# Kernel optimization log

Hardware: AMD Instinct MI355X
Metric: run time of the kernel (lower is better)

The kernel has to match this reference:

```python
import jax, jax.numpy as jnp
import numpy as np

NUM_CLASSES = 21
THRESH = 0.5
NEGPOS = 3
VAR0, VAR1 = 0.1, 0.2
FEAT = 19
N_ANCH = 9
B = 256
NUM_OBJS = 12
P = FEAT * FEAT * N_ANCH  # 3249


def make_priors():
    # 19x19 grid, 3 scales x 3 aspect ratios (1, 2, 1/2) -> 9 anchors/cell, center form
    cxy = (np.arange(FEAT, dtype=np.float32) + 0.5) / FEAT
    cx, cy = np.meshgrid(cxy, cxy, indexing='ij')  # [19,19]
    scales = np.array([0.1, 0.2, 0.35], dtype=np.float32)
    ratios = np.array([1.0, 2.0, 0.5], dtype=np.float32)
    w = (scales[:, None] * np.sqrt(ratios)[None, :]).reshape(-1)  # [9]
    h = (scales[:, None] / np.sqrt(ratios)[None, :]).reshape(-1)
    cx = np.broadcast_to(cx[:, :, None], (FEAT, FEAT, N_ANCH))
    cy = np.broadcast_to(cy[:, :, None], (FEAT, FEAT, N_ANCH))
    w = np.broadcast_to(w[None, None, :], (FEAT, FEAT, N_ANCH))
    h = np.broadcast_to(h[None, None, :], (FEAT, FEAT, N_ANCH))
    pri = np.stack([cx, cy, w, h], axis=-1).reshape(-1, 4)
    return jnp.asarray(np.clip(pri, 1e-3, 1.0))


def setup_inputs() -> dict:
    key = jax.random.key(0)
    k1, k2, k3, k4, k5 = jax.random.split(key, 5)
    loc_data = jax.random.normal(k1, (B, P, 4), dtype=jnp.float32)
    conf_data = jax.random.normal(k2, (B, P, NUM_CLASSES), dtype=jnp.float32)
    priors = make_priors()
    xy = jax.random.uniform(k3, (B, NUM_OBJS, 2), minval=0.05, maxval=0.65)
    wh = jax.random.uniform(k4, (B, NUM_OBJS, 2), minval=0.05, maxval=0.30)
    labels = jax.random.randint(k5, (B, NUM_OBJS), 0, NUM_CLASSES - 1).astype(jnp.float32)
    targets = jnp.concatenate([xy, xy + wh, labels[..., None]], axis=-1)  # [B,O,5]
    return {"loc_data": loc_data, "conf_data": conf_data, "priors": priors, "targets": targets}


def point_form(boxes):  # (cx,cy,w,h) -> (x1,y1,x2,y2)
    return jnp.concatenate([boxes[:, :2] - boxes[:, 2:] / 2,
                            boxes[:, :2] + boxes[:, 2:] / 2], axis=1)


def jaccard(a, b):  # a: [n,4], b: [m,4] point form -> [n,m]
    lt = jnp.maximum(a[:, None, :2], b[None, :, :2])
    rb = jnp.minimum(a[:, None, 2:], b[None, :, 2:])
    inter = jnp.prod(jnp.clip(rb - lt, 0.0, None), axis=-1)
    area_a = jnp.prod(a[:, 2:] - a[:, :2], axis=-1)
    area_b = jnp.prod(b[:, 2:] - b[:, :2], axis=-1)
    return inter / (area_a[:, None] + area_b[None, :] - inter)


def encode(matched, priors):  # matched point-form [P,4], priors center-form [P,4]
    g_cxcy = ((matched[:, :2] + matched[:, 2:]) / 2 - priors[:, :2]) / (VAR0 * priors[:, 2:])
    g_wh = jnp.log((matched[:, 2:] - matched[:, :2]) / priors[:, 2:]) / VAR1
    return jnp.concatenate([g_cxcy, g_wh], axis=1)


def match_one(truths, labels, priors, priors_pt):
    overlaps = jaccard(truths, priors_pt)          # [O,P]
    best_prior_idx = jnp.argmax(overlaps, axis=1)  # [O]
    best_truth_ov = jnp.max(overlaps, axis=0)      # [P]
    best_truth_idx = jnp.argmax(overlaps, axis=0)  # [P]
    best_truth_ov = best_truth_ov.at[best_prior_idx].set(2.0)
    best_truth_idx = best_truth_idx.at[best_prior_idx].set(jnp.arange(truths.shape[0]))
    matches = truths[best_truth_idx]               # [P,4]
    conf = labels[best_truth_idx] + 1
    conf = jnp.where(best_truth_ov < THRESH, 0, conf)
    return encode(matches, priors), conf


def reference(loc_data, conf_data, priors, targets):
    truths = targets[:, :, :4]
    labels = targets[:, :, 4].astype(jnp.int32)
    priors_pt = point_form(priors)
    loc_t, conf_t = jax.vmap(lambda t, l: match_one(t, l, priors, priors_pt))(truths, labels)
    loc_t = jax.lax.stop_gradient(loc_t)
    conf_t = jax.lax.stop_gradient(conf_t)

    pos = conf_t > 0                                               # [B,P]
    # smooth L1 (sum) over matched priors
    d = loc_data - loc_t
    ad = jnp.abs(d)
    sl1 = jnp.where(ad < 1.0, 0.5 * d * d, ad - 0.5)
    loss_l = jnp.sum(sl1 * pos[..., None].astype(sl1.dtype))

    # per-prior CE = logsumexp - logit[target]
    lse = jax.nn.logsumexp(conf_data, axis=-1)                     # [B,P]
    gathered = jnp.take_along_axis(conf_data, conf_t[..., None], axis=2)[..., 0]
    ce = lse - gathered                                            # [B,P]

    # hard negative mining: double argsort rank of neg losses
    loss_c_mine = jnp.where(pos, 0.0, ce)
    loss_idx = jnp.argsort(-loss_c_mine, axis=1)
    idx_rank = jnp.argsort(loss_idx, axis=1)
    num_pos = jnp.sum(pos, axis=1, keepdims=True)                  # [B,1]
    num_neg = jnp.minimum(NEGPOS * num_pos, P - 1)
    neg = idx_rank < num_neg

    sel = pos | neg
    loss_c = jnp.sum(jnp.where(sel, ce, 0.0))

    have_centerloss = jnp.max(sel.reshape(B, FEAT, FEAT, N_ANCH), axis=3).reshape(-1)
    conf_t_featuremap = jnp.max(conf_t.reshape(B, FEAT, FEAT, N_ANCH), axis=3).reshape(-1)

    N = jnp.sum(num_pos).astype(loc_data.dtype)
    return loss_l / N, loss_c / N, conf_t_featuremap, have_centerloss
```

## Files before the change

### kernel.cpp

```cpp
#include <hip/hip_runtime.h>
#include <math.h>

#pragma clang fp contract(off)

#define BB      256
#define PP      3249
#define NCLS    21
#define NOBJ    12
#define CELLS   361
#define CH      13
#define THRESH_ 0.5f

typedef float vf4 __attribute__((ext_vector_type(4), aligned(4)));
typedef float vrec __attribute__((ext_vector_type(4)));


struct Row { vf4 a, b, c, d, e; float f; };

__device__ __forceinline__ Row load_row(const float* cd) {
    const vf4* q = (const vf4*)cd;
    Row r;
    r.a = q[0]; r.b = q[1]; r.c = q[2]; r.d = q[3]; r.e = q[4];
    r.f = cd[20];
    return r;
}

__device__ __forceinline__ float lse21(const Row& r) {
    float m = r.a[0];
    m = fmaxf(m, r.a[1]); m = fmaxf(m, r.a[2]); m = fmaxf(m, r.a[3]);
    m = fmaxf(m, r.b[0]); m = fmaxf(m, r.b[1]); m = fmaxf(m, r.b[2]); m = fmaxf(m, r.b[3]);
    m = fmaxf(m, r.c[0]); m = fmaxf(m, r.c[1]); m = fmaxf(m, r.c[2]); m = fmaxf(m, r.c[3]);
    m = fmaxf(m, r.d[0]); m = fmaxf(m, r.d[1]); m = fmaxf(m, r.d[2]); m = fmaxf(m, r.d[3]);
    m = fmaxf(m, r.e[0]); m = fmaxf(m, r.e[1]); m = fmaxf(m, r.e[2]); m = fmaxf(m, r.e[3]);
    m = fmaxf(m, r.f);
    float s = 0.0f;
    s += expf(r.a[0]-m); s += expf(r.a[1]-m); s += expf(r.a[2]-m); s += expf(r.a[3]-m);
    s += expf(r.b[0]-m); s += expf(r.b[1]-m); s += expf(r.b[2]-m); s += expf(r.b[3]-m);
    s += expf(r.c[0]-m); s += expf(r.c[1]-m); s += expf(r.c[2]-m); s += expf(r.c[3]-m);
    s += expf(r.d[0]-m); s += expf(r.d[1]-m); s += expf(r.d[2]-m); s += expf(r.d[3]-m);
    s += expf(r.e[0]-m); s += expf(r.e[1]-m); s += expf(r.e[2]-m); s += expf(r.e[3]-m);
    s += expf(r.f-m);
    return logf(s) + m;
}

template <int NBITS>
__device__ __forceinline__ void agg_add(int* hist, bool active, unsigned bin, int lane) {
    unsigned long long mm = __ballot(active);
#pragma unroll
    for (int bit = 0; bit < NBITS; ++bit) {
        unsigned long long bb = __ballot(active && ((bin >> bit) & 1));
        mm &= ((bin >> bit) & 1) ? bb : ~bb;
    }
    if (active && (__ffsll(mm) - 1 == lane))
        atomicAdd(&hist[bin], (int)__popcll(mm));
}

__device__ __forceinline__ void pick_bin(const int* hist, int nbins, int kv, int lane,
                                         int* s_chosen, int* s_knext, int* s_cnt) {
    const int per = (nbins >= 64) ? (nbins >> 6) : 1;
    const int base = lane * per;
    int ls = 0;
    if (base < nbins)
        for (int k = 0; k < per; ++k) ls += hist[base + k];
    int x = ls;
#pragma unroll
    for (int off = 1; off < 64; off <<= 1) {
        int y = __shfl_down(x, off);
        if (lane + off < 64) x += y;
    }
    int cum = x - ls;
    if (base < nbins) {
        for (int k = per - 1; k >= 0; --k) {
            int h = hist[base + k];
            if (cum < kv && kv <= cum + h) { *s_chosen = base + k; *s_knext = kv - cum; *s_cnt = h; }
            cum += h;
        }
    }
}

__global__ __launch_bounds__(256, 6) void prep_kernel(
    const float* __restrict__ conf, const float* __restrict__ priors,
    const float* __restrict__ targets, vrec* __restrict__ recs,
    unsigned long long* __restrict__ pt)
{
    const int chunk = blockIdx.x, b = blockIdx.y;
    const int tid = threadIdx.x, lane = tid & 63, wid = tid >> 6;
    const int p = chunk * 256 + tid;
    const bool valid = (p < PP);

    __shared__ float s_tx1[NOBJ], s_ty1[NOBJ], s_tx2[NOBJ], s_ty2[NOBJ], s_area[NOBJ];
    __shared__ unsigned long long s_wk[NOBJ][4];

    if (tid < NOBJ) {
        const float* t = targets + ((size_t)b * NOBJ + tid) * 5;
        float x1 = t[0], y1 = t[1], x2 = t[2], y2 = t[3];
        s_tx1[tid] = x1; s_ty1[tid] = y1; s_tx2[tid] = x2; s_ty2[tid] = y2;
        s_area[tid] = (x2 - x1) * (y2 - y1);
    }
    __syncthreads();

    vf4 pr = {0.0f, 0.0f, 0.0f, 0.0f};
    if (valid) pr = *(const vf4*)(priors + 4 * p);
    float px1 = pr[0] - pr[2] / 2.0f, py1 = pr[1] - pr[3] / 2.0f;
    float px2 = pr[0] + pr[2] / 2.0f, py2 = pr[1] + pr[3] / 2.0f;
    float area_p = (px2 - px1) * (py2 - py1);

    float bov = -1.0f; int bidx = 0;
#pragma unroll
    for (int j = 0; j < NOBJ; ++j) {
        float ltx = fmaxf(s_tx1[j], px1);
        float lty = fmaxf(s_ty1[j], py1);
        float rbx = fminf(s_tx2[j], px2);
        float rby = fminf(s_ty2[j], py2);
        float iw = fmaxf(rbx - ltx, 0.0f);
        float ih = fmaxf(rby - lty, 0.0f);
        float inter = iw * ih;
        float iou = inter / ((s_area[j] + area_p) - inter);
        if (iou > bov) { bov = iou; bidx = j; }
        unsigned long long k = valid
            ? (((unsigned long long)__float_as_uint(iou) << 32) | (0xFFFFFFFFu - (unsigned)p))
            : 0ull;
#pragma unroll
        for (int off = 32; off > 0; off >>= 1) {
            unsigned long long k2 = __shfl_xor(k, off);
            if (k2 > k) k = k2;
        }
        if (lane == 0) s_wk[j][wid] = k;
    }

    if (valid) {
        Row r = load_row(conf + ((size_t)b * PP + p) * NCLS);
        float lse = lse21(r);
        vrec rec;
        rec[0] = bov; rec[1] = __int_as_float(bidx); rec[2] = lse; rec[3] = r.a[0];
        recs[(size_t)b * PP + p] = rec;
    }
    __syncthreads();
    if (tid < NOBJ) {
        unsigned long long m = s_wk[tid][0];
#pragma unroll
        for (int w2 = 1; w2 < 4; ++w2) { unsigned long long v = s_wk[tid][w2]; if (v > m) m = v; }
        pt[((size_t)b * CH + chunk) * NOBJ + tid] = m;
    }
}

__global__ __launch_bounds__(1024, 4) void select_kernel(
    const float* __restrict__ loc, const float* __restrict__ conf,
    const float* __restrict__ priors, const float* __restrict__ targets,
    const vrec* __restrict__ recs, const unsigned long long* __restrict__ pt,
    int* __restrict__ numpos, double* __restrict__ lossl,
    double* __restrict__ lossc, float* __restrict__ out)
{
    const int b = blockIdx.x, tid = threadIdx.x;
    const int lane = tid & 63, wid = tid >> 6;

    __shared__ float s_tx1[NOBJ], s_ty1[NOBJ], s_tx2[NOBJ], s_ty2[NOBJ];
    __shared__ int   s_label[NOBJ], s_bpi[NOBJ];
    __shared__ unsigned s_key[PP];
    __shared__ float s_ce[PP];
    __shared__ unsigned char s_ct[PP];
    __shared__ int s_hist[2][256];
    __shared__ int s_chosen, s_knext, s_cnt, s_nneg;
    __shared__ double s_pl[16];
    __shared__ int    s_pn[16];
    __shared__ double s_pc[16];

    const vrec* rb = recs + (size_t)b * PP;
    vrec r0 = rb[tid];
    vrec r1 = rb[tid + 1024];
    vrec r2 = rb[tid + 2048];
    const bool h3 = (tid + 3072 < PP);
    vrec r3; if (h3) r3 = rb[tid + 3072];

    if (tid < NOBJ) {
        const float* t = targets + ((size_t)b * NOBJ + tid) * 5;
        s_tx1[tid] = t[0]; s_ty1[tid] = t[1]; s_tx2[tid] = t[2]; s_ty2[tid] = t[3];
        s_label[tid] = (int)t[4];
        const unsigned long long* q = pt + (size_t)b * CH * NOBJ + tid;
        unsigned long long m = q[0];
#pragma unroll
        for (int c2 = 1; c2 < CH; ++c2) {
            unsigned long long v = q[(size_t)c2 * NOBJ];
            if (v > m) m = v;
        }
        s_bpi[tid] = (int)(0xFFFFFFFFu - (unsigned)(m & 0xFFFFFFFFull));
    }
    for (int k = tid; k < 512; k += 1024) ((int*)s_hist)[k] = 0;
    __syncthreads();

    int bpi[NOBJ];
#pragma unroll
    for (int j = 0; j < NOBJ; ++j) bpi[j] = s_bpi[j];

    int my_pos = 0;
    double my_lossl = 0.0;
    const float* confb = conf + (size_t)b * PP * NCLS;

    auto body = [&](vrec r, int p) {
        float bov = r[0]; int bidx = __float_as_int(r[1]);
        float lse = r[2]; float c0 = r[3];
        int jov = -1;
#pragma unroll
        for (int j = 0; j < NOBJ; ++j) if (bpi[j] == p) jov = j;
        int idx; float ov;
        if (jov >= 0) { idx = jov; ov = 2.0f; }
        else          { idx = bidx; ov = bov; }
        int c = (ov < THRESH_) ? 0 : (s_label[idx] + 1);
        s_ct[p] = (unsigned char)c;

        float cdc = (c == 0) ? c0 : confb[(size_t)p * NCLS + c];
        float ce  = lse - cdc;
        s_ce[p] = ce;
        float v = (c > 0) ? 0.0f : ce;
        s_key[p] = __float_as_uint(v);

        if (c > 0) {
            ++my_pos;
            vf4 prr = *(const vf4*)(priors + 4 * p);
            float m0 = s_tx1[idx], m1 = s_ty1[idx], m2 = s_tx2[idx], m3 = s_ty2[idx];
            float g0 = ((m0 + m2) / 2.0f - prr[0]) / (0.1f * prr[2]);
            float g1 = ((m1 + m3) / 2.0f - prr[1]) / (0.1f * prr[3]);
            float g2 = logf((m2 - m0) / prr[2]) / 0.2f;
            float g3 = logf((m3 - m1) / prr[3]) / 0.2f;
            const float* ld = loc + ((size_t)b * PP + p) * 4;
            float d0 = ld[0] - g0, d1 = ld[1] - g1, d2 = ld[2] - g2, d3 = ld[3] - g3;
            float a0 = fabsf(d0), a1 = fabsf(d1), a2 = fabsf(d2), a3 = fabsf(d3);
            my_lossl += (double)((a0 < 1.0f) ? 0.5f * d0 * d0 : a0 - 0.5f);
            my_lossl += (double)((a1 < 1.0f) ? 0.5f * d1 * d1 : a1 - 0.5f);
            my_lossl += (double)((a2 < 1.0f) ? 0.5f * d2 * d2 : a2 - 0.5f);
            my_lossl += (double)((a3 < 1.0f) ? 0.5f * d3 * d3 : a3 - 0.5f);
        }
    };
    body(r0, tid); body(r1, tid + 1024); body(r2, tid + 2048);
    if (h3) body(r3, tid + 3072);

#pragma unroll
    for (int off = 32; off > 0; off >>= 1) {
        my_lossl += __shfl_down(my_lossl, off);
        my_pos   += __shfl_down(my_pos, off);
    }
    if (lane == 0) { s_pl[wid] = my_lossl; s_pn[wid] = my_pos; }
    __syncthreads();
    if (tid == 0) {
        double L = 0.0; int n = 0;
#pragma unroll
        for (int w2 = 0; w2 < 16; ++w2) { L += s_pl[w2]; n += s_pn[w2]; }
        lossl[b] = L; numpos[b] = n;
        s_nneg = min(3 * n, PP - 1);
    }

    unsigned prefix = 0u, pmask = 0u;
    int ptie = 0x7FFFFFFF;
    bool done = false;
    const int shifts[4] = {24, 16, 8, 0};
#pragma unroll
    for (int r = 0; r < 4; ++r) {
        if (!done) {
            const int sh = shifts[r];
            int* hist = s_hist[r & 1];
            for (int i = tid; i < PP; i += 1024) {
                unsigned key = s_key[i];
                agg_add<8>(hist, (key & pmask) == prefix, (key >> sh) & 0xFFu, lane);
            }
            __syncthreads();
            if (tid < 64) pick_bin(hist, 256, (r == 0) ? s_nneg : s_knext, lane,
                                   &s_chosen, &s_knext, &s_cnt);
            else { for (int k = tid - 64; k < 256; k += 960) s_hist[(r + 1) & 1][k] = 0; }
            __syncthreads();
            prefix |= ((unsigned)s_chosen) << sh;
            pmask  |= 0xFFu << sh;
            if (s_cnt == 1) done = true;
        }
    }

    if (!done && s_knext < s_cnt) {
        int* hist = s_hist[0];
        for (int i = tid; i < PP; i += 1024)
            agg_add<8>(hist, s_key[i] == prefix, ((4095u - (unsigned)i) >> 4) & 0xFFu, lane);
        __syncthreads();
        if (tid < 64) pick_bin(hist, 256, s_knext, lane, &s_chosen, &s_knext, &s_cnt);
        else { for (int k = tid - 64; k < 256; k += 960) s_hist[1][k] = 0; }
        __syncthreads();
        const int binA = s_chosen;
        int* hist2 = s_hist[1];
        for (int i = tid; i < PP; i += 1024) {
            unsigned hi = 4095u - (unsigned)i;
            agg_add<4>(hist2, (s_key[i] == prefix) && (((hi >> 4) & 0xFFu) == (unsigned)binA),
                       hi & 0xFu, lane);
        }
        __syncthreads();
        if (tid < 64) pick_bin(hist2, 16, s_knext, lane, &s_chosen, &s_knext, &s_cnt);
        __syncthreads();
        ptie = 4095 - ((binA << 4) | s_chosen);
    }

    double my_c = 0.0;
    for (int cI = tid; cI < CELLS; cI += 1024) {
        int mc = 0, hv = 0;
#pragma unroll
        for (int a = 0; a < 9; ++a) {
            int p = cI * 9 + a;
            int cv = s_ct[p];
            unsigned km = s_key[p] & pmask;
            bool sel = (cv > 0) || (km > prefix) || (km == prefix && p <= ptie);
            mc = (cv > mc) ? cv : mc;
            hv |= sel ? 1 : 0;
            if (sel) my_c += (double)s_ce[p];
        }
        out[2 + (size_t)b * CELLS + cI] = (float)mc;
        out[2 + (size_t)BB * CELLS + (size_t)b * CELLS + cI] = (float)hv;
    }

#pragma unroll
    for (int off = 32; off > 0; off >>= 1) my_c += __shfl_down(my_c, off);
    if (lane == 0) s_pc[wid] = my_c;
    __syncthreads();
    if (tid == 0) {
        double L = 0.0;
#pragma unroll
        for (int w2 = 0; w2 < 16; ++w2) L += s_pc[w2];
        lossc[b] = L;
    }
}

__global__ __launch_bounds__(256) void finalize_kernel(
    const int* __restrict__ numpos, const double* __restrict__ lossl,
    const double* __restrict__ lossc, float* __restrict__ out)
{
    __shared__ double s_l[256], s_c[256];
    __shared__ int s_n[256];
    int tid = threadIdx.x;
    s_n[tid] = numpos[tid];
    s_l[tid] = lossl[tid];
    s_c[tid] = lossc[tid];
    __syncthreads();
    for (int s = 128; s > 0; s >>= 1) {
        if (tid < s) { s_n[tid] += s_n[tid + s]; s_l[tid] += s_l[tid + s]; s_c[tid] += s_c[tid + s]; }
        __syncthreads();
    }
    if (tid == 0) {
        double N = (double)s_n[0];
        out[0] = (float)(s_l[0] / N);
        out[1] = (float)(s_c[0] / N);
    }
}

extern "C" void kernel_launch(void* const* d_in, const int* in_sizes, int n_in,
                              void* d_out, int out_size, void* d_ws, size_t ws_size,
                              hipStream_t stream) {
    const float* loc     = (const float*)d_in[0];
    const float* conf    = (const float*)d_in[1];
    const float* priors  = (const float*)d_in[2];
    const float* targets = (const float*)d_in[3];
    float* out = (float*)d_out;

    double* ws_lossl  = (double*)d_ws;
    double* ws_lossc  = ws_lossl + BB;
    int*    ws_numpos = (int*)(ws_lossc + BB);
    unsigned long long* ws_pt = (unsigned long long*)(ws_numpos + BB);
    vrec*   ws_rec    = (vrec*)(ws_pt + (size_t)BB * CH * NOBJ);

    hipLaunchKernelGGL(prep_kernel, dim3(CH, BB), dim3(256), 0, stream,
                       conf, priors, targets, ws_rec, ws_pt);
    hipLaunchKernelGGL(select_kernel, dim3(BB), dim3(1024), 0, stream,
                       loc, conf, priors, targets, ws_rec, ws_pt,
                       ws_numpos, ws_lossl, ws_lossc, out);
    hipLaunchKernelGGL(finalize_kernel, dim3(1), dim3(256), 0, stream,
                       ws_numpos, ws_lossl, ws_lossc, out);
}
```

Measured before the change: 142.7 us.

## Fuse finalize into select via last-block atomic, hoist conf load, cheaper argmax shuffle

Removes the separate finalize kernel: each select block bumps an atomic counter after a threadfence, and the last block reduces the per-batch sums and writes the two scalar losses. The prep kernel now issues the conf row and prior loads before the targets barrier so their latency overlaps the IoU loop, with launch bounds relaxed from 6 to 4 to leave room for the extra live registers. The per-object 64-bit key shuffle-max is replaced by a float shuffle-max plus a ballot to find the lowest winning lane. These changes save one kernel launch and some shuffle work, at the cost of register pressure and a serial tail in the last block.

```diff
diff --git a/kernel.cpp b/kernel.cpp
--- a/kernel.cpp
+++ b/kernel.cpp
@@ -78,18 +78,24 @@
     }
 }
 
-__global__ __launch_bounds__(256, 6) void prep_kernel(
+__global__ __launch_bounds__(256, 4) void prep_kernel(
     const float* __restrict__ conf, const float* __restrict__ priors,
     const float* __restrict__ targets, vrec* __restrict__ recs,
-    unsigned long long* __restrict__ pt)
+    unsigned long long* __restrict__ pt, int* __restrict__ done)
 {
     const int chunk = blockIdx.x, b = blockIdx.y;
     const int tid = threadIdx.x, lane = tid & 63, wid = tid >> 6;
     const int p = chunk * 256 + tid;
     const bool valid = (p < PP);
 
+    if (chunk == 0 && b == 0 && tid == 0) *done = 0;
+
     __shared__ float s_tx1[NOBJ], s_ty1[NOBJ], s_tx2[NOBJ], s_ty2[NOBJ], s_area[NOBJ];
     __shared__ unsigned long long s_wk[NOBJ][4];
+
+    vf4 pr = {0.0f, 0.0f, 0.0f, 0.0f};
+    if (valid) pr = *(const vf4*)(priors + 4 * p);
+    Row r = load_row(conf + ((size_t)b * PP + (valid ? p : 0)) * NCLS);
 
     if (tid < NOBJ) {
         const float* t = targets + ((size_t)b * NOBJ + tid) * 5;
@@ -99,8 +105,6 @@
     }
     __syncthreads();
 
-    vf4 pr = {0.0f, 0.0f, 0.0f, 0.0f};
-    if (valid) pr = *(const vf4*)(priors + 4 * p);
     float px1 = pr[0] - pr[2] / 2.0f, py1 = pr[1] - pr[3] / 2.0f;
     float px2 = pr[0] + pr[2] / 2.0f, py2 = pr[1] + pr[3] / 2.0f;
     float area_p = (px2 - px1) * (py2 - py1);
@@ -117,19 +121,19 @@
         float inter = iw * ih;
         float iou = inter / ((s_area[j] + area_p) - inter);
         if (iou > bov) { bov = iou; bidx = j; }
-        unsigned long long k = valid
-            ? (((unsigned long long)__float_as_uint(iou) << 32) | (0xFFFFFFFFu - (unsigned)p))
-            : 0ull;
-#pragma unroll
-        for (int off = 32; off > 0; off >>= 1) {
-            unsigned long long k2 = __shfl_xor(k, off);
-            if (k2 > k) k = k2;
-        }
-        if (lane == 0) s_wk[j][wid] = k;
+        float m = iou;
+#pragma unroll
+        for (int off = 32; off > 0; off >>= 1)
+            m = fmaxf(m, __shfl_xor(m, off));
+        unsigned long long win = __ballot(iou == m);
+        if (lane == 0) {
+            int pw = chunk * 256 + wid * 64 + (__ffsll(win) - 1);
+            s_wk[j][wid] = ((unsigned long long)__float_as_uint(m) << 32)
+                         | (0xFFFFFFFFu - (unsigned)pw);
+        }
     }
 
     if (valid) {
-        Row r = load_row(conf + ((size_t)b * PP + p) * NCLS);
         float lse = lse21(r);
         vrec rec;
         rec[0] = bov; rec[1] = __int_as_float(bidx); rec[2] = lse; rec[3] = r.a[0];
@@ -149,7 +153,7 @@
     const float* __restrict__ priors, const float* __restrict__ targets,
     const vrec* __restrict__ recs, const unsigned long long* __restrict__ pt,
     int* __restrict__ numpos, double* __restrict__ lossl,
-    double* __restrict__ lossc, float* __restrict__ out)
+    double* __restrict__ lossc, int* __restrict__ done, float* __restrict__ out)
 {
     const int b = blockIdx.x, tid = threadIdx.x;
     const int lane = tid & 63, wid = tid >> 6;
@@ -160,10 +164,12 @@
     __shared__ float s_ce[PP];
     __shared__ unsigned char s_ct[PP];
     __shared__ int s_hist[2][256];
-    __shared__ int s_chosen, s_knext, s_cnt, s_nneg;
+    __shared__ int s_chosen, s_knext, s_cnt, s_nneg, s_last;
     __shared__ double s_pl[16];
     __shared__ int    s_pn[16];
     __shared__ double s_pc[16];
+    __shared__ double s_fl[4], s_fc[4];
+    __shared__ int    s_fn[4];
 
     const vrec* rb = recs + (size_t)b * PP;
     vrec r0 = rb[tid];
@@ -251,11 +257,11 @@
 
     unsigned prefix = 0u, pmask = 0u;
     int ptie = 0x7FFFFFFF;
-    bool done = false;
+    bool done_sel = false;
     const int shifts[4] = {24, 16, 8, 0};
 #pragma unroll
     for (int r = 0; r < 4; ++r) {
-        if (!done) {
+        if (!done_sel) {
             const int sh = shifts[r];
             int* hist = s_hist[r & 1];
             for (int i = tid; i < PP; i += 1024) {
@@ -269,11 +275,11 @@
             __syncthreads();
             prefix |= ((unsigned)s_chosen) << sh;
             pmask  |= 0xFFu << sh;
-            if (s_cnt == 1) done = true;
-        }
-    }
-
-    if (!done && s_knext < s_cnt) {
+            if (s_cnt == 1) done_sel = true;
+        }
+    }
+
+    if (!done_sel && s_knext < s_cnt) {
         int* hist = s_hist[0];
         for (int i = tid; i < PP; i += 1024)
             agg_add<8>(hist, s_key[i] == prefix, ((4095u - (unsigned)i) >> 4) & 0xFFu, lane);
@@ -320,28 +326,32 @@
 #pragma unroll
         for (int w2 = 0; w2 < 16; ++w2) L += s_pc[w2];
         lossc[b] = L;
-    }
-}
-
-__global__ __launch_bounds__(256) void finalize_kernel(
-    const int* __restrict__ numpos, const double* __restrict__ lossl,
-    const double* __restrict__ lossc, float* __restrict__ out)
-{
-    __shared__ double s_l[256], s_c[256];
-    __shared__ int s_n[256];
-    int tid = threadIdx.x;
-    s_n[tid] = numpos[tid];
-    s_l[tid] = lossl[tid];
-    s_c[tid] = lossc[tid];
-    __syncthreads();
-    for (int s = 128; s > 0; s >>= 1) {
-        if (tid < s) { s_n[tid] += s_n[tid + s]; s_l[tid] += s_l[tid + s]; s_c[tid] += s_c[tid + s]; }
-        __syncthreads();
-    }
-    if (tid == 0) {
-        double N = (double)s_n[0];
-        out[0] = (float)(s_l[0] / N);
-        out[1] = (float)(s_c[0] / N);
+        __threadfence();
+        int prev = atomicAdd(done, 1);
+        s_last = (prev == BB - 1) ? 1 : 0;
+    }
+    __syncthreads();
+
+    if (s_last) {
+        double fl = 0.0, fc = 0.0; int fn = 0;
+        if (tid < BB) { fl = lossl[tid]; fc = lossc[tid]; fn = numpos[tid]; }
+        if (tid < BB) {
+#pragma unroll
+            for (int off = 32; off > 0; off >>= 1) {
+                fl += __shfl_down(fl, off);
+                fc += __shfl_down(fc, off);
+                fn += __shfl_down(fn, off);
+            }
+            if (lane == 0) { s_fl[wid] = fl; s_fc[wid] = fc; s_fn[wid] = fn; }
+        }
+        __syncthreads();
+        if (tid == 0) {
+            double L = s_fl[0] + s_fl[1] + s_fl[2] + s_fl[3];
+            double C = s_fc[0] + s_fc[1] + s_fc[2] + s_fc[3];
+            double N = (double)(s_fn[0] + s_fn[1] + s_fn[2] + s_fn[3]);
+            out[0] = (float)(L / N);
+            out[1] = (float)(C / N);
+        }
     }
 }
 
@@ -357,14 +367,13 @@
     double* ws_lossl  = (double*)d_ws;
     double* ws_lossc  = ws_lossl + BB;
     int*    ws_numpos = (int*)(ws_lossc + BB);
-    unsigned long long* ws_pt = (unsigned long long*)(ws_numpos + BB);
+    int*    ws_done   = ws_numpos + BB;
+    unsigned long long* ws_pt = (unsigned long long*)(ws_done + 4);
     vrec*   ws_rec    = (vrec*)(ws_pt + (size_t)BB * CH * NOBJ);
 
     hipLaunchKernelGGL(prep_kernel, dim3(CH, BB), dim3(256), 0, stream,
-                       conf, priors, targets, ws_rec, ws_pt);
+                       conf, priors, targets, ws_rec, ws_pt, ws_done);
     hipLaunchKernelGGL(select_kernel, dim3(BB), dim3(1024), 0, stream,
                        loc, conf, priors, targets, ws_rec, ws_pt,
-                       ws_numpos, ws_lossl, ws_lossc, out);
-    hipLaunchKernelGGL(finalize_kernel, dim3(1), dim3(256), 0, stream,
-                       ws_numpos, ws_lossl, ws_lossc, out);
-}
+                       ws_numpos, ws_lossl, ws_lossc, ws_done, out);
+}
```

Measured after the change: 141.9 us. About the same (-0.5%).
